# Optimization experiments

Hardware: AMD Instinct MI355X
Metric: run time of the kernel (lower is better)

The kernel has to match this reference:

```python
import jax, jax.numpy as jnp
import numpy as np
from jax import lax


def _batch_conv(x, w, b):
    # x: [B, Cin, H, W], w: [B, Cout, Cin, kh, kw], b: [B, Cout]
    # Per-sample conv (the torch code's groups=B grouped-conv trick),
    # expressed as vmap over the batch of an ordinary conv.
    def one(xi, wi):
        return lax.conv_general_dilated(
            xi[None], wi, window_strides=(1, 1), padding='SAME',
            dimension_numbers=('NCHW', 'OIHW', 'NCHW'))[0]
    y = jax.vmap(one)(x, w)                       # [B, Cout, H, W]
    return y + b[:, :, None, None]


def setup_inputs() -> dict:
    key = jax.random.key(0)
    ks = jax.random.split(key, 9)
    B, Cin, H, W = 32, 3, 64, 64
    NC = 10
    s = 0.05
    return {
        'x': jax.random.normal(ks[0], (B, Cin, H, W), jnp.float32),
        'conv1_weight': jax.random.normal(ks[1], (B, 64, Cin, 3, 3), jnp.float32) * s,
        'conv2_weight': jax.random.normal(ks[2], (B, 128, 64, 3, 3), jnp.float32) * s,
        'conv3_weight': jax.random.normal(ks[3], (B, 256, 128, 3, 3), jnp.float32) * s,
        'fc_weight': jax.random.normal(ks[4], (B, 1, NC), jnp.float32) * s,
        'bias1': jax.random.normal(ks[5], (B, 64), jnp.float32) * s,
        'bias2': jax.random.normal(ks[6], (B, 128), jnp.float32) * s,
        'bias3': jax.random.normal(ks[7], (B, 256), jnp.float32) * s,
        'bias4': jax.random.normal(ks[8], (B, NC), jnp.float32) * s,
    }


def reference(x, conv1_weight, conv2_weight, conv3_weight, fc_weight,
              bias1, bias2, bias3, bias4):
    h = jax.nn.relu(_batch_conv(x, conv1_weight, bias1))   # [B, 64, H, W]
    h = jax.nn.relu(_batch_conv(h, conv2_weight, bias2))   # [B, 128, H, W]
    h = jax.nn.relu(_batch_conv(h, conv3_weight, bias3))   # [B, 256, H, W]
    h = jnp.mean(h, axis=(2, 3))                           # AdaptiveAvgPool2d(1) -> [B, 256]
    h = h[:, :, None]                                      # view(B, N, -1) -> [B, 256, 1]
    # BatchLinearLayer: bmm(x, weight) + bias
    out = jnp.einsum('bnd,bdo->bno', h, fc_weight) + bias4[:, None, :]  # [B, 256, 10]
    return out
```

## Files before the change

kernel.cpp:

```cpp
#include <hip/hip_runtime.h>
#include <stdint.h>

typedef __attribute__((ext_vector_type(8))) short short8;
typedef __attribute__((ext_vector_type(16))) float f32x16;

#define NB 32

__device__ __forceinline__ float bf2f(uint16_t v) {
    return __uint_as_float(((uint32_t)v) << 16);
}
__device__ __forceinline__ uint16_t f2bf(float f) {
    uint32_t u = __float_as_uint(f);
    u += 0x7fffu + ((u >> 16) & 1u);
    return (uint16_t)(u >> 16);
}

__device__ __forceinline__ void gload16(const void* g, void* l) {
    __builtin_amdgcn_global_load_lds(
        (const __attribute__((address_space(1))) uint32_t*)g,
        (__attribute__((address_space(3))) uint32_t*)l, 16, 0, 0);
}

template<int COUT, int CIN>
__device__ __forceinline__ void prep_w_item(int idx, const float* __restrict__ w,
                                            uint16_t* __restrict__ wp)
{
    const int ci = idx % CIN;
    const int t  = idx / CIN;
    const int oc = t % COUT;
    const int b  = t / COUT;
    const float* s = w + (size_t)idx * 9;
    #pragma unroll
    for (int k = 0; k < 9; k++)
        wp[((size_t)(b * 9 + k) * COUT + oc) * CIN + ci] = f2bf(s[k]);
}

__global__ __launch_bounds__(256) void prep_w3_k(
    const float* __restrict__ w, uint16_t* __restrict__ wp)
{
    const int idx = blockIdx.x * 256 + threadIdx.x;
    if (idx < NB * 256 * 128) prep_w_item<256, 128>(idx, w, wp);
}

template<bool DO_W3>
__global__ __launch_bounds__(256) void prep_all(
    const float* __restrict__ x,  const float* __restrict__ w1,
    const float* __restrict__ w2, const float* __restrict__ w3,
    uint16_t* __restrict__ xp,  uint16_t* __restrict__ wp1,
    uint16_t* __restrict__ wp2, uint16_t* __restrict__ wp3,
    float* __restrict__ zp)
{
    int idx = blockIdx.x * 256 + threadIdx.x;
    if (idx < 4096) {
        ((float4*)zp)[idx] = make_float4(0.f, 0.f, 0.f, 0.f);
        return;
    }
    idx -= 4096;
    if (idx < 131072) {
        const int xc = idx & 63, y = (idx >> 6) & 63, b = idx >> 12;
        const float* s = x + (size_t)b * 3 * 4096 + y * 64 + xc;
        const uint16_t v0 = f2bf(s[0]), v1 = f2bf(s[4096]), v2 = f2bf(s[8192]);
        short8 lo = {(short)v0, (short)v1, (short)v2, 0, 0, 0, 0, 0};
        short8 hi = {0, 0, 0, 0, 0, 0, 0, 0};
        uint16_t* d = xp + (size_t)idx * 16;
        *(short8*)d = lo;
        *(short8*)(d + 8) = hi;
        return;
    }
    idx -= 131072;
    if (idx < 18432) {
        const int oc = idx & 63, k = (idx >> 6) % 9, b = idx / 576;
        const uint16_t v0 = f2bf(w1[((size_t)(b * 64 + oc) * 3 + 0) * 9 + k]);
        const uint16_t v1 = f2bf(w1[((size_t)(b * 64 + oc) * 3 + 1) * 9 + k]);
        const uint16_t v2 = f2bf(w1[((size_t)(b * 64 + oc) * 3 + 2) * 9 + k]);
        short8 lo = {(short)v0, (short)v1, (short)v2, 0, 0, 0, 0, 0};
        short8 hi = {0, 0, 0, 0, 0, 0, 0, 0};
        uint16_t* d = wp1 + ((size_t)(b * 9 + k) * 64 + oc) * 16;
        *(short8*)d = lo;
        *(short8*)(d + 8) = hi;
        return;
    }
    idx -= 18432;
    if (idx < 262144) {
        prep_w_item<128, 64>(idx, w2, wp2);
        return;
    }
    if (!DO_W3) return;
    idx -= 262144;
    if (idx < 1048576) prep_w_item<256, 128>(idx, w3, wp3);
}

template<int CIN, int COUT, int OCBLKS, bool POOL>
__global__ __launch_bounds__(256, 2) void conv_mfma(
    const uint16_t* __restrict__ in, const uint16_t* __restrict__ wp,
    const float* __restrict__ bias, uint16_t* __restrict__ out,
    float* __restrict__ partial, const float* __restrict__ zp)
{
    constexpr int IN_GA = 1344;
    constexpr int W_G   = 1152;
    constexpr int IN_B  = IN_GA * 16;
    constexpr int BUF_B = IN_B + W_G * 16;
    constexpr int P     = OCBLKS * 8;
    extern __shared__ __align__(16) char sm[];

    const int L   = blockIdx.x;
    const int xcd = L & 7;
    const int jj  = L >> 3;
    const int b   = (jj / P) * 8 + xcd;
    const int inner = jj % P;
    const int ocbase = (inner >> 3) * 64;
    const int stripe = inner & 7;
    const int y0 = stripe * 8;

    const int tid = threadIdx.x;
    const int wv = tid >> 6, l = tid & 63, q = l >> 5, ln = l & 31;
    const int NK = CIN / 16;

    const uint16_t* src_in[6];
    #pragma unroll
    for (int i = 0; i < 6; i++) {
        const int gp = i * 256 + tid;
        const int g = gp ^ ((gp >> 3) & 7);
        const int qq = g & 1, site = g >> 1;
        const int row = site / 66, px = site - row * 66;
        const int gy = y0 - 1 + row, gx = px - 1;
        const bool valid = (row < 10) && ((unsigned)gy < 64u) && ((unsigned)gx < 64u);
        src_in[i] = valid ? in + ((size_t)((b * 64 + gy) * 64 + gx) * CIN + qq * 8)
                          : (const uint16_t*)zp;
    }
    const uint16_t* src_w[5];
    #pragma unroll
    for (int i = 0; i < 5; i++) {
        const int gp = i * 256 + tid;
        const int g = gp ^ ((gp >> 3) & 7);
        const int qq = g & 1, kk = g >> 7, oc = (g >> 1) & 63;
        src_w[i] = wp + ((size_t)(b * 9 + kk) * COUT + ocbase + oc) * CIN + qq * 8;
    }

    int aoff[4][3][2];
    #pragma unroll
    for (int t = 0; t < 4; t++)
        #pragma unroll
        for (int kx = 0; kx < 3; kx++)
            #pragma unroll
            for (int h = 0; h < 2; h++) {
                const int g = ((wv * 2 + t) * 66 + h * 32 + ln + kx) * 2 + q;
                aoff[t][kx][h] = (g ^ ((g >> 3) & 7)) * 16;
            }
    const int gb = ln * 2 + q;
    const int boff = (gb ^ ((gb >> 3) & 7)) * 16;

    f32x16 aA0, aA1, aB0, aB1, aC0, aC1, aD0, aD1;
    {
        const float bv0 = bias[b * COUT + ocbase + ln];
        const float bv1 = bias[b * COUT + ocbase + 32 + ln];
        #pragma unroll
        for (int r = 0; r < 16; r++) {
            aA0[r] = bv0; aB0[r] = bv0; aC0[r] = bv0; aD0[r] = bv0;
            aA1[r] = bv1; aB1[r] = bv1; aC1[r] = bv1; aD1[r] = bv1;
        }
    }

    auto stage = [&](char* base, int k) {
        const int koff = k * 16;
        #pragma unroll
        for (int i = 0; i < 6; i++) {
            const int g0 = i * 256 + wv * 64;
            if (g0 < IN_GA) gload16(src_in[i] + koff, base + g0 * 16);
        }
        #pragma unroll
        for (int i = 0; i < 5; i++) {
            const int g0 = i * 256 + wv * 64;
            if (g0 < W_G) gload16(src_w[i] + koff, base + IN_B + g0 * 16);
        }
    };

    stage(sm, 0);
    asm volatile("s_waitcnt vmcnt(0)" ::: "memory");
    __syncthreads();

    for (int k = 0; k < NK; k++) {
        char* cb = sm + (k & 1) * BUF_B;
        if (k + 1 < NK) stage(sm + ((k + 1) & 1) * BUF_B, k + 1);
        __builtin_amdgcn_s_setprio(1);
        #pragma unroll
        for (int ky = 0; ky < 3; ky++)
            #pragma unroll
            for (int kx = 0; kx < 3; kx++) {
                const int kk = ky * 3 + kx;
                short8 fA = *(const short8*)(cb + aoff[ky + 0][kx][0]);
                short8 fB = *(const short8*)(cb + aoff[ky + 0][kx][1]);
                short8 fC = *(const short8*)(cb + aoff[ky + 1][kx][0]);
                short8 fD = *(const short8*)(cb + aoff[ky + 1][kx][1]);
                const char* bw = cb + IN_B + kk * 2048 + boff;
                short8 b0 = *(const short8*)(bw);
                short8 b1 = *(const short8*)(bw + 1024);
                aA0 = __builtin_amdgcn_mfma_f32_32x32x16_bf16(fA, b0, aA0, 0, 0, 0);
                aB0 = __builtin_amdgcn_mfma_f32_32x32x16_bf16(fB, b0, aB0, 0, 0, 0);
                aC0 = __builtin_amdgcn_mfma_f32_32x32x16_bf16(fC, b0, aC0, 0, 0, 0);
                aD0 = __builtin_amdgcn_mfma_f32_32x32x16_bf16(fD, b0, aD0, 0, 0, 0);
                aA1 = __builtin_amdgcn_mfma_f32_32x32x16_bf16(fA, b1, aA1, 0, 0, 0);
                aB1 = __builtin_amdgcn_mfma_f32_32x32x16_bf16(fB, b1, aB1, 0, 0, 0);
                aC1 = __builtin_amdgcn_mfma_f32_32x32x16_bf16(fC, b1, aC1, 0, 0, 0);
                aD1 = __builtin_amdgcn_mfma_f32_32x32x16_bf16(fD, b1, aD1, 0, 0, 0);
            }
        __builtin_amdgcn_s_setprio(0);
        asm volatile("s_waitcnt vmcnt(0)" ::: "memory");
        __syncthreads();
    }

    if (!POOL) {
        #pragma unroll
        for (int r = 0; r < 16; r++) {
            const int pxr = (r & 3) + 8 * (r >> 2) + 4 * q;
            const int y0w = y0 + wv * 2;
            uint16_t* dA = out + (size_t)((b * 64 + y0w) * 64 + pxr) * COUT + ocbase;
            uint16_t* dB = out + (size_t)((b * 64 + y0w) * 64 + 32 + pxr) * COUT + ocbase;
            uint16_t* dC = out + (size_t)((b * 64 + y0w + 1) * 64 + pxr) * COUT + ocbase;
            uint16_t* dD = out + (size_t)((b * 64 + y0w + 1) * 64 + 32 + pxr) * COUT + ocbase;
            dA[ln]      = f2bf(fmaxf(aA0[r], 0.f));
            dA[32 + ln] = f2bf(fmaxf(aA1[r], 0.f));
            dB[ln]      = f2bf(fmaxf(aB0[r], 0.f));
            dB[32 + ln] = f2bf(fmaxf(aB1[r], 0.f));
            dC[ln]      = f2bf(fmaxf(aC0[r], 0.f));
            dC[32 + ln] = f2bf(fmaxf(aC1[r], 0.f));
            dD[ln]      = f2bf(fmaxf(aD0[r], 0.f));
            dD[32 + ln] = f2bf(fmaxf(aD1[r], 0.f));
        }
    } else {
        float* red = (float*)(sm + 2 * BUF_B);
        float s0 = 0.f, s1 = 0.f;
        #pragma unroll
        for (int r = 0; r < 16; r++) {
            s0 += fmaxf(aA0[r], 0.f) + fmaxf(aB0[r], 0.f)
                + fmaxf(aC0[r], 0.f) + fmaxf(aD0[r], 0.f);
            s1 += fmaxf(aA1[r], 0.f) + fmaxf(aB1[r], 0.f)
                + fmaxf(aC1[r], 0.f) + fmaxf(aD1[r], 0.f);
        }
        s0 += __shfl_xor(s0, 32);
        s1 += __shfl_xor(s1, 32);
        if (q == 0) {
            red[wv * 64 + ln] = s0;
            red[wv * 64 + 32 + ln] = s1;
        }
        __syncthreads();
        if (tid < 64) {
            float t = red[tid] + red[64 + tid] + red[128 + tid] + red[192 + tid];
            partial[(size_t)(b * 256 + ocbase + tid) * 8 + stripe] = t;
        }
    }
}

__global__ void fc_k(const float* __restrict__ partial,
                     const float* __restrict__ fcw,
                     const float* __restrict__ b4, float* __restrict__ out)
{
    const int b = blockIdx.x, c = threadIdx.x;
    const float* p = partial + (size_t)(b * 256 + c) * 8;
    float s = 0.f;
    #pragma unroll
    for (int i = 0; i < 8; i++) s += p[i];
    const float pooled = s * (1.f / 4096.f);
    #pragma unroll
    for (int o = 0; o < 10; o++)
        out[(b * 256 + c) * 10 + o] = fmaf(pooled, fcw[b * 10 + o], b4[b * 10 + o]);
}

extern "C" void kernel_launch(void* const* d_in, const int* in_sizes, int n_in,
                              void* d_out, int out_size, void* d_ws, size_t ws_size,
                              hipStream_t stream)
{
    const float* x   = (const float*)d_in[0];
    const float* w1  = (const float*)d_in[1];
    const float* w2  = (const float*)d_in[2];
    const float* w3  = (const float*)d_in[3];
    const float* fcw = (const float*)d_in[4];
    const float* b1  = (const float*)d_in[5];
    const float* b2  = (const float*)d_in[6];
    const float* b3  = (const float*)d_in[7];
    const float* b4  = (const float*)d_in[8];
    char* ws = (char*)d_ws;
    uint16_t* xp  = (uint16_t*)(ws);
    uint16_t* wp1 = (uint16_t*)(ws + 4194304);
    uint16_t* h2  = (uint16_t*)(ws);
    uint16_t* h1  = (uint16_t*)(ws + 33554432);
    uint16_t* wp2 = (uint16_t*)(ws + 50331648);
    const bool big_ws = ws_size >= 74186752u;
    uint16_t* wp3     = (uint16_t*)(ws + (big_ws ? 55050240u : 33554432u));
    float*    partial = (float*)   (ws + (big_ws ? 73924608u : 52428800u));
    float*    zp      = (float*)d_out;

    constexpr int DYN_LDS = 2 * 39936 + 1024;
    static bool attr_done = false;
    if (!attr_done) {
        hipFuncSetAttribute((const void*)&conv_mfma<16, 64, 1, false>,
                            hipFuncAttributeMaxDynamicSharedMemorySize, DYN_LDS);
        hipFuncSetAttribute((const void*)&conv_mfma<64, 128, 2, false>,
                            hipFuncAttributeMaxDynamicSharedMemorySize, DYN_LDS);
        hipFuncSetAttribute((const void*)&conv_mfma<128, 256, 4, true>,
                            hipFuncAttributeMaxDynamicSharedMemorySize, DYN_LDS);
        attr_done = true;
    }

    if (big_ws) {
        prep_all<true><<<5720, 256, 0, stream>>>(x, w1, w2, w3, xp, wp1, wp2, wp3, zp);
    } else {
        prep_all<false><<<1624, 256, 0, stream>>>(x, w1, w2, w3, xp, wp1, wp2, wp3, zp);
    }
    conv_mfma<16, 64, 1, false><<<NB * 8, 256, DYN_LDS, stream>>>(xp, wp1, b1, h1, nullptr, zp);
    conv_mfma<64, 128, 2, false><<<NB * 16, 256, DYN_LDS, stream>>>(h1, wp2, b2, h2, nullptr, zp);
    if (!big_ws)
        prep_w3_k<<<4096, 256, 0, stream>>>(w3, wp3);
    conv_mfma<128, 256, 4, true><<<NB * 32, 256, DYN_LDS, stream>>>(h2, wp3, b3, nullptr, partial, zp);
    fc_k<<<NB, 256, 0, stream>>>(partial, fcw, b4, (float*)d_out);
}
```

Baseline: 119.8 us.

## Prefetch two stages ahead with uniform per-wave load counts and partial vmcnt waits

Reorganizes the global-to-LDS staging so each wave issues exactly 10 loads per stage, padding unused slots with dummy loads into a scratch LDS area. This makes the count of outstanding loads the same for every wave, so the loop can wait with vmcnt(10) and keep the next stage's loads in flight. It issues stage k+2 into the buffer just consumed, after a barrier, which lets the loads overlap the MFMA work more deeply. The cost is an extra 1 KB of LDS for the dummy target and the pooling scratch, plus wasted dummy loads.

```diff
diff --git a/kernel.cpp b/kernel.cpp
--- a/kernel.cpp
+++ b/kernel.cpp
@@ -96,10 +96,10 @@
     const float* __restrict__ bias, uint16_t* __restrict__ out,
     float* __restrict__ partial, const float* __restrict__ zp)
 {
-    constexpr int IN_GA = 1344;
-    constexpr int W_G   = 1152;
-    constexpr int IN_B  = IN_GA * 16;
-    constexpr int BUF_B = IN_B + W_G * 16;
+    constexpr int IN_CH = 21;
+    constexpr int W_CH  = 18;
+    constexpr int IN_B  = IN_CH * 1024;
+    constexpr int BUF_B = IN_B + W_CH * 1024;
     constexpr int P     = OCBLKS * 8;
     extern __shared__ __align__(16) char sm[];
 
@@ -116,25 +116,31 @@
     const int wv = tid >> 6, l = tid & 63, q = l >> 5, ln = l & 31;
     const int NK = CIN / 16;
 
-    const uint16_t* src_in[6];
-    #pragma unroll
-    for (int i = 0; i < 6; i++) {
-        const int gp = i * 256 + tid;
-        const int g = gp ^ ((gp >> 3) & 7);
-        const int qq = g & 1, site = g >> 1;
-        const int row = site / 66, px = site - row * 66;
-        const int gy = y0 - 1 + row, gx = px - 1;
-        const bool valid = (row < 10) && ((unsigned)gy < 64u) && ((unsigned)gx < 64u);
-        src_in[i] = valid ? in + ((size_t)((b * 64 + gy) * 64 + gx) * CIN + qq * 8)
-                          : (const uint16_t*)zp;
-    }
-    const uint16_t* src_w[5];
-    #pragma unroll
-    for (int i = 0; i < 5; i++) {
-        const int gp = i * 256 + tid;
-        const int g = gp ^ ((gp >> 3) & 7);
-        const int qq = g & 1, kk = g >> 7, oc = (g >> 1) & 63;
-        src_w[i] = wp + ((size_t)(b * 9 + kk) * COUT + ocbase + oc) * CIN + qq * 8;
+    const uint16_t* srcp[10];
+    int ldsoff[10];
+    #pragma unroll
+    for (int j = 0; j < 10; j++) {
+        const int chunk = wv * 10 + j;
+        if (chunk >= IN_CH + W_CH) {
+            srcp[j] = (const uint16_t*)zp;
+            ldsoff[j] = -1;
+        } else if (chunk < IN_CH) {
+            const int gp = chunk * 64 + l;
+            const int g = gp ^ ((gp >> 3) & 7);
+            const int qq = g & 1, site = g >> 1;
+            const int row = site / 66, px = site - row * 66;
+            const int gy = y0 - 1 + row, gx = px - 1;
+            const bool valid = (row < 10) && ((unsigned)gy < 64u) && ((unsigned)gx < 64u);
+            srcp[j] = valid ? in + ((size_t)((b * 64 + gy) * 64 + gx) * CIN + qq * 8)
+                            : (const uint16_t*)zp;
+            ldsoff[j] = chunk * 1024;
+        } else {
+            const int gp = (chunk - IN_CH) * 64 + l;
+            const int g = gp ^ ((gp >> 3) & 7);
+            const int qq = g & 1, kk = g >> 7, oc = (g >> 1) & 63;
+            srcp[j] = wp + ((size_t)(b * 9 + kk) * COUT + ocbase + oc) * CIN + qq * 8;
+            ldsoff[j] = IN_B + (chunk - IN_CH) * 1024;
+        }
     }
 
     int aoff[4][3][2];
@@ -161,27 +167,26 @@
         }
     }
 
-    auto stage = [&](char* base, int k) {
+    auto stage = [&](int bufsel, int k) {
         const int koff = k * 16;
-        #pragma unroll
-        for (int i = 0; i < 6; i++) {
-            const int g0 = i * 256 + wv * 64;
-            if (g0 < IN_GA) gload16(src_in[i] + koff, base + g0 * 16);
-        }
-        #pragma unroll
-        for (int i = 0; i < 5; i++) {
-            const int g0 = i * 256 + wv * 64;
-            if (g0 < W_G) gload16(src_w[i] + koff, base + IN_B + g0 * 16);
+        char* base = sm + bufsel * BUF_B;
+        #pragma unroll
+        for (int j = 0; j < 10; j++) {
+            char* dst = (ldsoff[j] < 0) ? (sm + 2 * BUF_B)
+                                        : (base + ldsoff[j]);
+            gload16(srcp[j] + koff, dst);
         }
     };
 
-    stage(sm, 0);
-    asm volatile("s_waitcnt vmcnt(0)" ::: "memory");
-    __syncthreads();
+    stage(0, 0);
+    if (NK > 1) stage(1, 1);
 
     for (int k = 0; k < NK; k++) {
-        char* cb = sm + (k & 1) * BUF_B;
-        if (k + 1 < NK) stage(sm + ((k + 1) & 1) * BUF_B, k + 1);
+        const char* cb = sm + (k & 1) * BUF_B;
+        if (k + 1 < NK) asm volatile("s_waitcnt vmcnt(10)" ::: "memory");
+        else            asm volatile("s_waitcnt vmcnt(0)"  ::: "memory");
+        __builtin_amdgcn_s_barrier();
+        __builtin_amdgcn_sched_barrier(0);
         __builtin_amdgcn_s_setprio(1);
         #pragma unroll
         for (int ky = 0; ky < 3; ky++)
@@ -205,8 +210,8 @@
                 aD1 = __builtin_amdgcn_mfma_f32_32x32x16_bf16(fD, b1, aD1, 0, 0, 0);
             }
         __builtin_amdgcn_s_setprio(0);
-        asm volatile("s_waitcnt vmcnt(0)" ::: "memory");
-        __syncthreads();
+        __builtin_amdgcn_s_barrier();
+        if (k + 2 < NK) stage(k & 1, k + 2);
     }
 
     if (!POOL) {
@@ -228,7 +233,7 @@
             dD[32 + ln] = f2bf(fmaxf(aD1[r], 0.f));
         }
     } else {
-        float* red = (float*)(sm + 2 * BUF_B);
+        float* red = (float*)(sm + 2 * BUF_B + 1024);
         float s0 = 0.f, s1 = 0.f;
         #pragma unroll
         for (int r = 0; r < 16; r++) {
@@ -290,7 +295,7 @@
     float*    partial = (float*)   (ws + (big_ws ? 73924608u : 52428800u));
     float*    zp      = (float*)d_out;
 
-    constexpr int DYN_LDS = 2 * 39936 + 1024;
+    constexpr int DYN_LDS = 2 * 39936 + 1024 + 1024;
     static bool attr_done = false;
     if (!attr_done) {
         hipFuncSetAttribute((const void*)&conv_mfma<16, 64, 1, false>,
```

Measured after the change: 122.4 us. 1.02x slower.

## Drop LDS XOR swizzle for plane-major layout and software-pipeline fragment loads

Applied to the files above, without the earlier changes.

Changes the LDS staging layout for input halo and weight tiles from an XOR-swizzled interleaved form to a plane-major form where each 16-channel half occupies a contiguous plane, so the kx shift becomes a simple +16 byte offset and fewer address registers are needed. Adds a one-step software pipeline in the 9-tap loop that loads the next tap's LDS fragments before issuing the current tap's MFMAs, separated by a sched_barrier. This aims to hide LDS latency behind MFMA work and reduce register pressure. Removing the swizzle may add LDS bank conflicts, and double-buffering the fragments raises VGPR use.

```diff
diff --git a/kernel.cpp b/kernel.cpp
--- a/kernel.cpp
+++ b/kernel.cpp
@@ -120,11 +120,10 @@
     #pragma unroll
     for (int i = 0; i < 6; i++) {
         const int gp = i * 256 + tid;
-        const int g = gp ^ ((gp >> 3) & 7);
-        const int qq = g & 1, site = g >> 1;
-        const int row = site / 66, px = site - row * 66;
+        const int rq = gp / 66, px = gp - rq * 66;
+        const int row = rq >> 1, qq = rq & 1;
         const int gy = y0 - 1 + row, gx = px - 1;
-        const bool valid = (row < 10) && ((unsigned)gy < 64u) && ((unsigned)gx < 64u);
+        const bool valid = (rq < 20) && ((unsigned)gy < 64u) && ((unsigned)gx < 64u);
         src_in[i] = valid ? in + ((size_t)((b * 64 + gy) * 64 + gx) * CIN + qq * 8)
                           : (const uint16_t*)zp;
     }
@@ -132,23 +131,18 @@
     #pragma unroll
     for (int i = 0; i < 5; i++) {
         const int gp = i * 256 + tid;
-        const int g = gp ^ ((gp >> 3) & 7);
-        const int qq = g & 1, kk = g >> 7, oc = (g >> 1) & 63;
+        const int kq = gp >> 6, oc = gp & 63;
+        const int kk = kq >> 1, qq = kq & 1;
         src_w[i] = wp + ((size_t)(b * 9 + kk) * COUT + ocbase + oc) * CIN + qq * 8;
     }
 
-    int aoff[4][3][2];
+    int aoff[4][2];
     #pragma unroll
     for (int t = 0; t < 4; t++)
         #pragma unroll
-        for (int kx = 0; kx < 3; kx++)
-            #pragma unroll
-            for (int h = 0; h < 2; h++) {
-                const int g = ((wv * 2 + t) * 66 + h * 32 + ln + kx) * 2 + q;
-                aoff[t][kx][h] = (g ^ ((g >> 3) & 7)) * 16;
-            }
-    const int gb = ln * 2 + q;
-    const int boff = (gb ^ ((gb >> 3) & 7)) * 16;
+        for (int h = 0; h < 2; h++)
+            aoff[t][h] = ((((wv * 2 + t) * 2 + q) * 66) + h * 32 + ln) * 16;
+    const int qoff = q * 1024 + ln * 16;
 
     f32x16 aA0, aA1, aB0, aB1, aC0, aC1, aD0, aD1;
     {
@@ -180,30 +174,41 @@
     __syncthreads();
 
     for (int k = 0; k < NK; k++) {
-        char* cb = sm + (k & 1) * BUF_B;
+        const char* cb = sm + (k & 1) * BUF_B;
         if (k + 1 < NK) stage(sm + ((k + 1) & 1) * BUF_B, k + 1);
+
+        auto lda = [&](int kk, short8& fA, short8& fB, short8& fC, short8& fD,
+                       short8& b0, short8& b1) {
+            const int ky = kk / 3, kx = kk % 3;
+            fA = *(const short8*)(cb + aoff[ky][0] + kx * 16);
+            fB = *(const short8*)(cb + aoff[ky][1] + kx * 16);
+            fC = *(const short8*)(cb + aoff[ky + 1][0] + kx * 16);
+            fD = *(const short8*)(cb + aoff[ky + 1][1] + kx * 16);
+            const char* bw = cb + IN_B + kk * 2048 + qoff;
+            b0 = *(const short8*)(bw);
+            b1 = *(const short8*)(bw + 512);
+        };
+
+        short8 cA, cB2, cC, cD, c0, c1;
+        lda(0, cA, cB2, cC, cD, c0, c1);
         __builtin_amdgcn_s_setprio(1);
         #pragma unroll
-        for (int ky = 0; ky < 3; ky++)
-            #pragma unroll
-            for (int kx = 0; kx < 3; kx++) {
-                const int kk = ky * 3 + kx;
-                short8 fA = *(const short8*)(cb + aoff[ky + 0][kx][0]);
-                short8 fB = *(const short8*)(cb + aoff[ky + 0][kx][1]);
-                short8 fC = *(const short8*)(cb + aoff[ky + 1][kx][0]);
-                short8 fD = *(const short8*)(cb + aoff[ky + 1][kx][1]);
-                const char* bw = cb + IN_B + kk * 2048 + boff;
-                short8 b0 = *(const short8*)(bw);
-                short8 b1 = *(const short8*)(bw + 1024);
-                aA0 = __builtin_amdgcn_mfma_f32_32x32x16_bf16(fA, b0, aA0, 0, 0, 0);
-                aB0 = __builtin_amdgcn_mfma_f32_32x32x16_bf16(fB, b0, aB0, 0, 0, 0);
-                aC0 = __builtin_amdgcn_mfma_f32_32x32x16_bf16(fC, b0, aC0, 0, 0, 0);
-                aD0 = __builtin_amdgcn_mfma_f32_32x32x16_bf16(fD, b0, aD0, 0, 0, 0);
-                aA1 = __builtin_amdgcn_mfma_f32_32x32x16_bf16(fA, b1, aA1, 0, 0, 0);
-                aB1 = __builtin_amdgcn_mfma_f32_32x32x16_bf16(fB, b1, aB1, 0, 0, 0);
-                aC1 = __builtin_amdgcn_mfma_f32_32x32x16_bf16(fC, b1, aC1, 0, 0, 0);
-                aD1 = __builtin_amdgcn_mfma_f32_32x32x16_bf16(fD, b1, aD1, 0, 0, 0);
+        for (int kk = 0; kk < 9; kk++) {
+            short8 nA, nB2, nC, nD, n0, n1;
+            if (kk < 8) lda(kk + 1, nA, nB2, nC, nD, n0, n1);
+            __builtin_amdgcn_sched_barrier(0);
+            aA0 = __builtin_amdgcn_mfma_f32_32x32x16_bf16(cA, c0, aA0, 0, 0, 0);
+            aB0 = __builtin_amdgcn_mfma_f32_32x32x16_bf16(cB2, c0, aB0, 0, 0, 0);
+            aC0 = __builtin_amdgcn_mfma_f32_32x32x16_bf16(cC, c0, aC0, 0, 0, 0);
+            aD0 = __builtin_amdgcn_mfma_f32_32x32x16_bf16(cD, c0, aD0, 0, 0, 0);
+            aA1 = __builtin_amdgcn_mfma_f32_32x32x16_bf16(cA, c1, aA1, 0, 0, 0);
+            aB1 = __builtin_amdgcn_mfma_f32_32x32x16_bf16(cB2, c1, aB1, 0, 0, 0);
+            aC1 = __builtin_amdgcn_mfma_f32_32x32x16_bf16(cC, c1, aC1, 0, 0, 0);
+            aD1 = __builtin_amdgcn_mfma_f32_32x32x16_bf16(cD, c1, aD1, 0, 0, 0);
+            if (kk < 8) {
+                cA = nA; cB2 = nB2; cC = nC; cD = nD; c0 = n0; c1 = n1;
             }
+        }
         __builtin_amdgcn_s_setprio(0);
         asm volatile("s_waitcnt vmcnt(0)" ::: "memory");
         __syncthreads();
```

Result: slower. 129.5 us (+8.1%).
